# Kernel tuning notes

Hardware: AMD Instinct MI355X
Metric: run time of the kernel (lower is better)

The kernel has to match this reference:

```python
import jax, jax.numpy as jnp
import numpy as np

N, E, DIN, DOUT = 40000, 640000, 128, 256
BN_EPS = 1e-5  # torch BatchNorm1d default eps


def setup_inputs() -> dict:
    key = jax.random.key(0)
    ks = jax.random.split(key, 16)
    x = jax.random.normal(ks[0], (N, DIN), jnp.float32)
    edge_index = jax.random.randint(ks[1], (2, E), 0, N, dtype=jnp.int32)
    s1 = 1.0 / np.sqrt(DIN)
    s2 = 1.0 / np.sqrt(DOUT)
    return {
        "x": x,
        "edge_index": edge_index,
        "eps": jnp.zeros((), jnp.float32),  # GINConv train_eps init = 0
        "W1": jax.random.normal(ks[2], (DIN, DOUT), jnp.float32) * s1,
        "b1": jnp.zeros((DOUT,), jnp.float32),
        "g1": jnp.ones((DOUT,), jnp.float32),
        "bt1": jnp.zeros((DOUT,), jnp.float32),
        "m1": jax.random.normal(ks[3], (DOUT,), jnp.float32) * 0.1,
        "v1": jax.random.uniform(ks[4], (DOUT,), jnp.float32, 0.5, 1.5),
        "W2": jax.random.normal(ks[5], (DOUT, DOUT), jnp.float32) * s2,
        "b2": jnp.zeros((DOUT,), jnp.float32),
        "g2": jnp.ones((DOUT,), jnp.float32),
        "bt2": jnp.zeros((DOUT,), jnp.float32),
        "m2": jax.random.normal(ks[6], (DOUT,), jnp.float32) * 0.1,
        "v2": jax.random.uniform(ks[7], (DOUT,), jnp.float32, 0.5, 1.5),
        "Wres": jax.random.normal(ks[8], (DIN, DOUT), jnp.float32) * s1,
    }


def _bn(h, g, b, m, v):
    # inference-mode BatchNorm1d with running stats
    return (h - m) * jax.lax.rsqrt(v + BN_EPS) * g + b


def reference(x, edge_index, eps, W1, b1, g1, bt1, m1, v1,
              W2, b2, g2, bt2, m2, v2, Wres):
    src, dst = edge_index[0], edge_index[1]
    # GIN sum aggregation: messages x[src] scatter-added at dst
    agg = jax.ops.segment_sum(x[src], dst, num_segments=N)  # [N, DIN]
    h = (1.0 + eps) * x + agg
    h = jax.nn.relu(_bn(h @ W1 + b1, g1, bt1, m1, v1))       # [N, DOUT]
    h = jax.nn.relu(_bn(h @ W2 + b2, g2, bt2, m2, v2))       # [N, DOUT]
    # dropout is identity in eval mode; residual projection since DIN != DOUT
    return jax.nn.relu(h + x @ Wres)
```

## Files before the change

kernel.cpp:

```cpp
#include <hip/hip_runtime.h>

#define NN 40000
#define NPAD 40064
#define EE 640000
#define KDIN 128
#define KDOUT 256

#define NBIN 157
#define BCAP 5120
#define HCAP 2816

typedef __attribute__((ext_vector_type(8))) short bf16x8;
typedef __attribute__((ext_vector_type(4))) float f32x4;

static __device__ __forceinline__ unsigned short f2bf(float f) {
    union { float f; unsigned int u; } v; v.f = f;
    unsigned int r = (v.u + 0x7FFFu + ((v.u >> 16) & 1u)) >> 16;
    return (unsigned short)r;
}
static __device__ __forceinline__ float bf2f(unsigned short h) {
    union { unsigned int u; float f; } v; v.u = ((unsigned int)h) << 16;
    return v.f;
}

#define FRONT_GRID 3177
__global__ __launch_bounds__(256) void k_front(
    const float* __restrict__ x,
    const float* __restrict__ W1, const float* __restrict__ W2,
    const float* __restrict__ Wres, const int* __restrict__ ei,
    ushort* __restrict__ xb, ushort* __restrict__ wt_all,
    unsigned int* __restrict__ recs, int* __restrict__ lmat,
    ushort* __restrict__ hb) {
    __shared__ unsigned int SM[4096 + 480 + 256];
    int b = blockIdx.x, tid = threadIdx.x;
    if (b < NBIN) {
        unsigned int* lrec = SM;
        int* cnt    = (int*)(SM + 4096);
        int* lstart = cnt + 160;
        int* lcur   = lstart + 160;
        int* sw     = lcur + 160;
        int e0 = b * 4096;
        int ns = min(e0 + 4096, EE) - e0;

        if (tid < NBIN) cnt[tid] = 0;
        __syncthreads();
        for (int s = tid; s < ns; s += 256)
            atomicAdd(&cnt[ei[EE + e0 + s] >> 8], 1);
        __syncthreads();
        sw[tid] = (tid < NBIN) ? cnt[tid] : 0;
        __syncthreads();
        for (int off = 1; off < 256; off <<= 1) {
            int add = (tid >= off) ? sw[tid - off] : 0;
            __syncthreads();
            sw[tid] += add;
            __syncthreads();
        }
        if (tid < NBIN) {
            int st = sw[tid] - cnt[tid];
            lstart[tid] = st;
            lcur[tid] = st;
        }
        __syncthreads();
        for (int s = tid; s < ns; s += 256) {
            int e = e0 + s;
            int src = ei[e];
            int dst = ei[EE + e];
            int p = atomicAdd(&lcur[dst >> 8], 1);
            lrec[p] = ((unsigned int)(dst & 255) << 16) | (unsigned int)src;
        }
        __syncthreads();
        for (int s = tid; s < ns; s += 256)
            recs[b * 4096 + s] = lrec[s];
        if (tid < NBIN + 1)
            lmat[b * 158 + tid] = (tid < NBIN) ? lstart[tid] : ns;
    } else if (b < 2661) {
        int i = (b - NBIN) * 256 + tid;
        int row = i >> 4;
        uint4 o = {0, 0, 0, 0};
        if (row < NN) {
            const float4* xp = (const float4*)x + (size_t)i * 2;
            float4 a = xp[0], c = xp[1];
            o.x = (unsigned)f2bf(a.x) | ((unsigned)f2bf(a.y) << 16);
            o.y = (unsigned)f2bf(a.z) | ((unsigned)f2bf(a.w) << 16);
            o.z = (unsigned)f2bf(c.x) | ((unsigned)f2bf(c.y) << 16);
            o.w = (unsigned)f2bf(c.z) | ((unsigned)f2bf(c.w) << 16);
        }
        if (row < NPAD) *(uint4*)(xb + (size_t)i * 8) = o;
    } else if (b < 3173) {
        int j = (b - 2661) * 256 + tid;
        if (j < 32768) {
            int c = j >> 7, r = j & 127;
            wt_all[j] = f2bf(W1[r * KDOUT + c]);
        } else if (j < 98304) {
            int j2 = j - 32768;
            int c = j2 >> 8, r = j2 & 255;
            wt_all[j] = f2bf(W2[r * KDOUT + c]);
        } else {
            int j3 = j - 98304;
            int c = j3 >> 7, r = j3 & 127;
            wt_all[j] = f2bf(Wres[r * KDOUT + c]);
        }
    } else {
        int idx = (b - 3173) * 256 + tid;
        ((uint4*)(hb + (size_t)NN * KDIN))[idx] = (uint4){0, 0, 0, 0};
    }
}

__global__ __launch_bounds__(256) void k_aggD(
    const unsigned int* __restrict__ recs, const int* __restrict__ lmat,
    const ushort* __restrict__ xb, const float* __restrict__ eps,
    ushort* __restrict__ hb) {
    __shared__ unsigned int lrec[BCAP];
    __shared__ ushort lsrc[HCAP];
    __shared__ int lcnt[128], lst[128], lcur[128];
    __shared__ int sw[256];
    int tid = threadIdx.x;
    int bi = blockIdx.x;
    int b = bi >> 3, nh = (bi >> 2) & 1, q = bi & 3;
    int wid = tid >> 6, lane = tid & 63;

    int len0 = 0;
    if (tid < NBIN) len0 = lmat[tid * 158 + b + 1] - lmat[tid * 158 + b];
    sw[tid] = len0;
    __syncthreads();
    for (int off = 1; off < 256; off <<= 1) {
        int add = (tid >= off) ? sw[tid - off] : 0;
        __syncthreads();
        sw[tid] += add;
        __syncthreads();
    }
    int ctot = sw[255];

    for (int c = wid; c < NBIN; c += 4) {
        int s0 = lmat[c * 158 + b];
        int len = lmat[c * 158 + b + 1] - s0;
        int pofs = sw[c] - len;
        const unsigned int* seg = recs + c * 4096 + s0;
        for (int i = lane; i < len; i += 64)
            lrec[pofs + i] = seg[i];
    }
    if (tid < 128) lcnt[tid] = 0;
    __syncthreads();

    for (int s = tid; s < ctot; s += 256) {
        int d8 = lrec[s] >> 16;
        if ((d8 >> 7) == nh) atomicAdd(&lcnt[d8 & 127], 1);
    }
    __syncthreads();
    sw[tid] = (tid < 128) ? lcnt[tid] : 0;
    __syncthreads();
    for (int off = 1; off < 128; off <<= 1) {
        int add = (tid >= off) ? sw[tid - off] : 0;
        __syncthreads();
        sw[tid] += add;
        __syncthreads();
    }
    if (tid < 128) {
        int e = sw[tid] - lcnt[tid];
        lst[tid] = e;
        lcur[tid] = e;
    }
    __syncthreads();
    for (int s = tid; s < ctot; s += 256) {
        unsigned int r = lrec[s];
        int d8 = r >> 16;
        if ((d8 >> 7) == nh) {
            int p = atomicAdd(&lcur[d8 & 127], 1);
            lsrc[p] = (ushort)(r & 0xffff);
        }
    }
    __syncthreads();

    int g = tid >> 2, lane4 = tid & 3;
    float s1 = 1.0f + eps[0];
    for (int it = 0; it < 2; ++it) {
        int d = g + it * 64;
        int node = b * 256 + nh * 128 + d;
        if (node >= NN) continue;
        int st = lst[d], en = st + lcnt[d];
        uint4 me = *((const uint4*)(xb + (size_t)node * KDIN) + q * 4 + lane4);
        float a[8], a2[8];
        a[0] = bf2f((ushort)(me.x & 0xffff)) * s1; a[1] = bf2f((ushort)(me.x >> 16)) * s1;
        a[2] = bf2f((ushort)(me.y & 0xffff)) * s1; a[3] = bf2f((ushort)(me.y >> 16)) * s1;
        a[4] = bf2f((ushort)(me.z & 0xffff)) * s1; a[5] = bf2f((ushort)(me.z >> 16)) * s1;
        a[6] = bf2f((ushort)(me.w & 0xffff)) * s1; a[7] = bf2f((ushort)(me.w >> 16)) * s1;
#pragma unroll
        for (int i = 0; i < 8; ++i) a2[i] = 0.f;
        int e = st;
        for (; e + 1 < en; e += 2) {
            int sA = lsrc[e], sB = lsrc[e + 1];
            uint4 v0 = *((const uint4*)(xb + (size_t)sA * KDIN) + q * 4 + lane4);
            uint4 v1 = *((const uint4*)(xb + (size_t)sB * KDIN) + q * 4 + lane4);
            a[0] += bf2f((ushort)(v0.x & 0xffff)); a[1] += bf2f((ushort)(v0.x >> 16));
            a[2] += bf2f((ushort)(v0.y & 0xffff)); a[3] += bf2f((ushort)(v0.y >> 16));
            a[4] += bf2f((ushort)(v0.z & 0xffff)); a[5] += bf2f((ushort)(v0.z >> 16));
            a[6] += bf2f((ushort)(v0.w & 0xffff)); a[7] += bf2f((ushort)(v0.w >> 16));
            a2[0] += bf2f((ushort)(v1.x & 0xffff)); a2[1] += bf2f((ushort)(v1.x >> 16));
            a2[2] += bf2f((ushort)(v1.y & 0xffff)); a2[3] += bf2f((ushort)(v1.y >> 16));
            a2[4] += bf2f((ushort)(v1.z & 0xffff)); a2[5] += bf2f((ushort)(v1.z >> 16));
            a2[6] += bf2f((ushort)(v1.w & 0xffff)); a2[7] += bf2f((ushort)(v1.w >> 16));
        }
        if (e < en) {
            int sA = lsrc[e];
            uint4 v0 = *((const uint4*)(xb + (size_t)sA * KDIN) + q * 4 + lane4);
            a[0] += bf2f((ushort)(v0.x & 0xffff)); a[1] += bf2f((ushort)(v0.x >> 16));
            a[2] += bf2f((ushort)(v0.y & 0xffff)); a[3] += bf2f((ushort)(v0.y >> 16));
            a[4] += bf2f((ushort)(v0.z & 0xffff)); a[5] += bf2f((ushort)(v0.z >> 16));
            a[6] += bf2f((ushort)(v0.w & 0xffff)); a[7] += bf2f((ushort)(v0.w >> 16));
        }
#pragma unroll
        for (int i = 0; i < 8; ++i) a[i] += a2[i];
        uint4 o;
        o.x = (unsigned)f2bf(a[0]) | ((unsigned)f2bf(a[1]) << 16);
        o.y = (unsigned)f2bf(a[2]) | ((unsigned)f2bf(a[3]) << 16);
        o.z = (unsigned)f2bf(a[4]) | ((unsigned)f2bf(a[5]) << 16);
        o.w = (unsigned)f2bf(a[6]) | ((unsigned)f2bf(a[7]) << 16);
        *((uint4*)(hb + (size_t)node * KDIN) + q * 4 + lane4) = o;
    }
}


#define STAGE_WT(Wt_, Kc_, K2_)                                                 \
    for (int id = tid; id < BNT * (K2_) / 16; id += 256) {                      \
        int c = id / ((K2_) / 16);                                              \
        int koff = (id % ((K2_) / 16)) * 16;                                    \
        uint4 v = *(const uint4*)((const char*)((Wt_) + (size_t)(ncol0 + c) * (Kc_)) + koff); \
        *(uint4*)((char*)s + c * (K2_) + (koff ^ ((c & 7) << 4))) = v;          \
    }

#define MM_LOOP(A_, Kc_, K2_, acc0_, acc1_)                                     \
    {                                                                           \
        const char* a0p = (const char*)((A_) + (size_t)r0 * (Kc_)) + lq * 16;   \
        const char* a1p = a0p + 16 * (Kc_) * 2;                                 \
        for (int k0 = 0; k0 < (Kc_); k0 += 32) {                                \
            bf16x8 a0 = *(const bf16x8*)(a0p + k0 * 2);                         \
            bf16x8 a1 = *(const bf16x8*)(a1p + k0 * 2);                         \
            int kb = (k0 + lq * 8) * 2;                                         \
            _Pragma("unroll")                                                   \
            for (int nt = 0; nt < 8; ++nt) {                                    \
                int c = nt * 16 + l15;                                          \
                bf16x8 b = *(const bf16x8*)((const char*)s + c * (K2_) + (kb ^ ((c & 7) << 4))); \
                acc0_[nt] = __builtin_amdgcn_mfma_f32_16x16x32_bf16(a0, b, acc0_[nt], 0, 0, 0); \
                acc1_[nt] = __builtin_amdgcn_mfma_f32_16x16x32_bf16(a1, b, acc1_[nt], 0, 0, 0); \
            }                                                                   \
        }                                                                       \
    }

#define BNT 128

__global__ __launch_bounds__(256) void k_mm1(
    const ushort* __restrict__ A, const ushort* __restrict__ Wt,
    const float* __restrict__ bb, const float* __restrict__ g,
    const float* __restrict__ bt, const float* __restrict__ m,
    const float* __restrict__ vv, ushort* __restrict__ C) {
    __shared__ ushort s[BNT * 128];
    int tid = threadIdx.x;
    int bm = blockIdx.x >> 1, bn = blockIdx.x & 1;
    int ncol0 = bn * BNT;
    STAGE_WT(Wt, 128, 256);
    __syncthreads();
    int wid = tid >> 6, lane = tid & 63;
    int l15 = lane & 15, lq = lane >> 4;
    int r0 = bm * 128 + wid * 32 + l15;
    f32x4 acc0[8] = {}, acc1[8] = {};
    MM_LOOP(A, 128, 256, acc0, acc1);
#pragma unroll
    for (int nt = 0; nt < 8; ++nt) {
        int col = ncol0 + nt * 16 + l15;
        float sc = g[col] * rsqrtf(vv[col] + 1e-5f);
        float bo = (bb[col] - m[col]) * sc + bt[col];
        int rb = bm * 128 + wid * 32 + lq * 4;
#pragma unroll
        for (int r = 0; r < 4; ++r) {
            C[(size_t)(rb + r) * KDOUT + col] = f2bf(fmaxf(acc0[nt][r] * sc + bo, 0.f));
            C[(size_t)(rb + 16 + r) * KDOUT + col] = f2bf(fmaxf(acc1[nt][r] * sc + bo, 0.f));
        }
    }
}

__global__ __launch_bounds__(256) void k_mm2(
    const ushort* __restrict__ H1, const ushort* __restrict__ W2t,
    const ushort* __restrict__ X, const ushort* __restrict__ Wrt,
    const float* __restrict__ bb, const float* __restrict__ g,
    const float* __restrict__ bt, const float* __restrict__ m,
    const float* __restrict__ vv, float* __restrict__ OUT) {
    __shared__ ushort s[BNT * 256];
    int tid = threadIdx.x;
    int bm = blockIdx.x >> 1, bn = blockIdx.x & 1;
    int ncol0 = bn * BNT;
    int wid = tid >> 6, lane = tid & 63;
    int l15 = lane & 15, lq = lane >> 4;
    int r0 = bm * 128 + wid * 32 + l15;

    STAGE_WT(W2t, 256, 512);
    __syncthreads();
    f32x4 acc0[8] = {}, acc1[8] = {};
    MM_LOOP(H1, 256, 512, acc0, acc1);

    __syncthreads();
    STAGE_WT(Wrt, 128, 256);
    __syncthreads();
    f32x4 acd0[8] = {}, acd1[8] = {};
    MM_LOOP(X, 128, 256, acd0, acd1);

#pragma unroll
    for (int nt = 0; nt < 8; ++nt) {
        int col = ncol0 + nt * 16 + l15;
        float sc = g[col] * rsqrtf(vv[col] + 1e-5f);
        float bo = (bb[col] - m[col]) * sc + bt[col];
        int rb = bm * 128 + wid * 32 + lq * 4;
#pragma unroll
        for (int r = 0; r < 4; ++r) {
            int row0 = rb + r, row1 = rb + 16 + r;
            float t0 = fmaxf(acc0[nt][r] * sc + bo, 0.f);
            float t1 = fmaxf(acc1[nt][r] * sc + bo, 0.f);
            if (row0 < NN) OUT[(size_t)row0 * KDOUT + col] = fmaxf(t0 + acd0[nt][r], 0.f);
            if (row1 < NN) OUT[(size_t)row1 * KDOUT + col] = fmaxf(t1 + acd1[nt][r], 0.f);
        }
    }
}

extern "C" void kernel_launch(void* const* d_in, const int* in_sizes, int n_in,
                              void* d_out, int out_size, void* d_ws, size_t ws_size,
                              hipStream_t stream) {
    const float* x    = (const float*)d_in[0];
    const int*   ei   = (const int*)d_in[1];
    const float* eps  = (const float*)d_in[2];
    const float* W1   = (const float*)d_in[3];
    const float* b1   = (const float*)d_in[4];
    const float* g1   = (const float*)d_in[5];
    const float* bt1  = (const float*)d_in[6];
    const float* m1   = (const float*)d_in[7];
    const float* v1   = (const float*)d_in[8];
    const float* W2   = (const float*)d_in[9];
    const float* b2   = (const float*)d_in[10];
    const float* g2   = (const float*)d_in[11];
    const float* bt2  = (const float*)d_in[12];
    const float* m2   = (const float*)d_in[13];
    const float* v2   = (const float*)d_in[14];
    const float* Wres = (const float*)d_in[15];
    float* out = (float*)d_out;

    char* w = (char*)d_ws;
    ushort* xb  = (ushort*)w;                 w += (size_t)NPAD * KDIN * 2;
    ushort* hb  = (ushort*)w;                 w += (size_t)NPAD * KDIN * 2;
    ushort* h1b = (ushort*)w;                 w += (size_t)NPAD * KDOUT * 2;
    ushort* w1t = (ushort*)w;                 w += 256 * 128 * 2;
    ushort* w2t = (ushort*)w;                 w += 256 * 256 * 2;
    ushort* wrt = (ushort*)w;                 w += 256 * 128 * 2;
    unsigned int* recs = (unsigned int*)w;    w += (size_t)NBIN * 4096 * 4;
    int* lmat   = (int*)w;                    w += (size_t)NBIN * 158 * 4;

    k_front<<<FRONT_GRID, 256, 0, stream>>>(x, W1, W2, Wres, ei, xb, w1t,
                                            recs, lmat, hb);
    k_aggD<<<NBIN * 8, 256, 0, stream>>>(recs, lmat, xb, eps, hb);

    const int grid = (NPAD / 128) * 2;
    k_mm1<<<grid, 256, 0, stream>>>(hb, w1t, b1, g1, bt1, m1, v1, h1b);
    k_mm2<<<grid, 256, 0, stream>>>(h1b, w2t, xb, wrt, b2, g2, bt2, m2, v2, out);
}
```

Baseline: 114.8 us.

## Unroll gather loop by four and use 256-row 512-thread tiles in mm2

The aggregation kernel now keeps four independent source-row loads in flight per iteration instead of two, using macros to trim the repeated code. The second matmul kernel launches 512-thread blocks covering 256 rows each, so the staged weight tile in shared memory is reused by twice as many rows. NPAD and the front-kernel grid are enlarged to match the 256-row tiling. Risks are higher register pressure and fewer blocks in mm2, which may lower occupancy or leave some compute units idle.

```diff
diff --git a/kernel.cpp b/kernel.cpp
--- a/kernel.cpp
+++ b/kernel.cpp
@@ -1,7 +1,7 @@
 #include <hip/hip_runtime.h>
 
 #define NN 40000
-#define NPAD 40064
+#define NPAD 40192
 #define EE 640000
 #define KDIN 128
 #define KDOUT 256
@@ -23,7 +23,7 @@
     return v.f;
 }
 
-#define FRONT_GRID 3177
+#define FRONT_GRID 3193
 __global__ __launch_bounds__(256) void k_front(
     const float* __restrict__ x,
     const float* __restrict__ W1, const float* __restrict__ W2,
@@ -73,7 +73,7 @@
             recs[b * 4096 + s] = lrec[s];
         if (tid < NBIN + 1)
             lmat[b * 158 + tid] = (tid < NBIN) ? lstart[tid] : ns;
-    } else if (b < 2661) {
+    } else if (b < 2669) {
         int i = (b - NBIN) * 256 + tid;
         int row = i >> 4;
         uint4 o = {0, 0, 0, 0};
@@ -85,9 +85,9 @@
             o.z = (unsigned)f2bf(c.x) | ((unsigned)f2bf(c.y) << 16);
             o.w = (unsigned)f2bf(c.z) | ((unsigned)f2bf(c.w) << 16);
         }
-        if (row < NPAD) *(uint4*)(xb + (size_t)i * 8) = o;
-    } else if (b < 3173) {
-        int j = (b - 2661) * 256 + tid;
+        *(uint4*)(xb + (size_t)i * 8) = o;
+    } else if (b < 3181) {
+        int j = (b - 2669) * 256 + tid;
         if (j < 32768) {
             int c = j >> 7, r = j & 127;
             wt_all[j] = f2bf(W1[r * KDOUT + c]);
@@ -101,10 +101,18 @@
             wt_all[j] = f2bf(Wres[r * KDOUT + c]);
         }
     } else {
-        int idx = (b - 3173) * 256 + tid;
+        int idx = (b - 3181) * 256 + tid;
         ((uint4*)(hb + (size_t)NN * KDIN))[idx] = (uint4){0, 0, 0, 0};
     }
 }
+
+#define ACC8(arr_, v_)                                                          \
+    arr_[0] += bf2f((ushort)((v_).x & 0xffff)); arr_[1] += bf2f((ushort)((v_).x >> 16)); \
+    arr_[2] += bf2f((ushort)((v_).y & 0xffff)); arr_[3] += bf2f((ushort)((v_).y >> 16)); \
+    arr_[4] += bf2f((ushort)((v_).z & 0xffff)); arr_[5] += bf2f((ushort)((v_).z >> 16)); \
+    arr_[6] += bf2f((ushort)((v_).w & 0xffff)); arr_[7] += bf2f((ushort)((v_).w >> 16));
+
+#define XROW(n_) (*((const uint4*)(xb + (size_t)(n_) * KDIN) + qoff))
 
 __global__ __launch_bounds__(256) void k_aggD(
     const unsigned int* __restrict__ recs, const int* __restrict__ lmat,
@@ -172,41 +180,35 @@
     __syncthreads();
 
     int g = tid >> 2, lane4 = tid & 3;
+    int qoff = q * 4 + lane4;
     float s1 = 1.0f + eps[0];
     for (int it = 0; it < 2; ++it) {
         int d = g + it * 64;
         int node = b * 256 + nh * 128 + d;
         if (node >= NN) continue;
         int st = lst[d], en = st + lcnt[d];
-        uint4 me = *((const uint4*)(xb + (size_t)node * KDIN) + q * 4 + lane4);
+        uint4 me = XROW(node);
         float a[8], a2[8];
-        a[0] = bf2f((ushort)(me.x & 0xffff)) * s1; a[1] = bf2f((ushort)(me.x >> 16)) * s1;
-        a[2] = bf2f((ushort)(me.y & 0xffff)) * s1; a[3] = bf2f((ushort)(me.y >> 16)) * s1;
-        a[4] = bf2f((ushort)(me.z & 0xffff)) * s1; a[5] = bf2f((ushort)(me.z >> 16)) * s1;
-        a[6] = bf2f((ushort)(me.w & 0xffff)) * s1; a[7] = bf2f((ushort)(me.w >> 16)) * s1;
 #pragma unroll
         for (int i = 0; i < 8; ++i) a2[i] = 0.f;
+        ACC8(a2, me);
+#pragma unroll
+        for (int i = 0; i < 8; ++i) { a[i] = a2[i] * s1; a2[i] = 0.f; }
         int e = st;
-        for (; e + 1 < en; e += 2) {
-            int sA = lsrc[e], sB = lsrc[e + 1];
-            uint4 v0 = *((const uint4*)(xb + (size_t)sA * KDIN) + q * 4 + lane4);
-            uint4 v1 = *((const uint4*)(xb + (size_t)sB * KDIN) + q * 4 + lane4);
-            a[0] += bf2f((ushort)(v0.x & 0xffff)); a[1] += bf2f((ushort)(v0.x >> 16));
-            a[2] += bf2f((ushort)(v0.y & 0xffff)); a[3] += bf2f((ushort)(v0.y >> 16));
-            a[4] += bf2f((ushort)(v0.z & 0xffff)); a[5] += bf2f((ushort)(v0.z >> 16));
-            a[6] += bf2f((ushort)(v0.w & 0xffff)); a[7] += bf2f((ushort)(v0.w >> 16));
-            a2[0] += bf2f((ushort)(v1.x & 0xffff)); a2[1] += bf2f((ushort)(v1.x >> 16));
-            a2[2] += bf2f((ushort)(v1.y & 0xffff)); a2[3] += bf2f((ushort)(v1.y >> 16));
-            a2[4] += bf2f((ushort)(v1.z & 0xffff)); a2[5] += bf2f((ushort)(v1.z >> 16));
-            a2[6] += bf2f((ushort)(v1.w & 0xffff)); a2[7] += bf2f((ushort)(v1.w >> 16));
-        }
-        if (e < en) {
-            int sA = lsrc[e];
-            uint4 v0 = *((const uint4*)(xb + (size_t)sA * KDIN) + q * 4 + lane4);
-            a[0] += bf2f((ushort)(v0.x & 0xffff)); a[1] += bf2f((ushort)(v0.x >> 16));
-            a[2] += bf2f((ushort)(v0.y & 0xffff)); a[3] += bf2f((ushort)(v0.y >> 16));
-            a[4] += bf2f((ushort)(v0.z & 0xffff)); a[5] += bf2f((ushort)(v0.z >> 16));
-            a[6] += bf2f((ushort)(v0.w & 0xffff)); a[7] += bf2f((ushort)(v0.w >> 16));
+        for (; e + 3 < en; e += 4) {
+            int sA = lsrc[e], sB = lsrc[e + 1], sC = lsrc[e + 2], sD = lsrc[e + 3];
+            uint4 v0 = XROW(sA);
+            uint4 v1 = XROW(sB);
+            uint4 v2 = XROW(sC);
+            uint4 v3 = XROW(sD);
+            ACC8(a, v0);
+            ACC8(a2, v1);
+            ACC8(a, v2);
+            ACC8(a2, v3);
+        }
+        for (; e < en; ++e) {
+            uint4 v0 = XROW(lsrc[e]);
+            ACC8(a, v0);
         }
 #pragma unroll
         for (int i = 0; i < 8; ++i) a[i] += a2[i];
@@ -215,13 +217,13 @@
         o.y = (unsigned)f2bf(a[2]) | ((unsigned)f2bf(a[3]) << 16);
         o.z = (unsigned)f2bf(a[4]) | ((unsigned)f2bf(a[5]) << 16);
         o.w = (unsigned)f2bf(a[6]) | ((unsigned)f2bf(a[7]) << 16);
-        *((uint4*)(hb + (size_t)node * KDIN) + q * 4 + lane4) = o;
-    }
-}
-
-
-#define STAGE_WT(Wt_, Kc_, K2_)                                                 \
-    for (int id = tid; id < BNT * (K2_) / 16; id += 256) {                      \
+        *((uint4*)(hb + (size_t)node * KDIN) + qoff) = o;
+    }
+}
+
+
+#define STAGE_WT(Wt_, Kc_, K2_, TPB_)                                           \
+    for (int id = tid; id < BNT * (K2_) / 16; id += (TPB_)) {                   \
         int c = id / ((K2_) / 16);                                              \
         int koff = (id % ((K2_) / 16)) * 16;                                    \
         uint4 v = *(const uint4*)((const char*)((Wt_) + (size_t)(ncol0 + c) * (Kc_)) + koff); \
@@ -257,7 +259,7 @@
     int tid = threadIdx.x;
     int bm = blockIdx.x >> 1, bn = blockIdx.x & 1;
     int ncol0 = bn * BNT;
-    STAGE_WT(Wt, 128, 256);
+    STAGE_WT(Wt, 128, 256, 256);
     __syncthreads();
     int wid = tid >> 6, lane = tid & 63;
     int l15 = lane & 15, lq = lane >> 4;
@@ -278,7 +280,7 @@
     }
 }
 
-__global__ __launch_bounds__(256) void k_mm2(
+__global__ __launch_bounds__(512) void k_mm2(
     const ushort* __restrict__ H1, const ushort* __restrict__ W2t,
     const ushort* __restrict__ X, const ushort* __restrict__ Wrt,
     const float* __restrict__ bb, const float* __restrict__ g,
@@ -290,15 +292,15 @@
     int ncol0 = bn * BNT;
     int wid = tid >> 6, lane = tid & 63;
     int l15 = lane & 15, lq = lane >> 4;
-    int r0 = bm * 128 + wid * 32 + l15;
-
-    STAGE_WT(W2t, 256, 512);
+    int r0 = bm * 256 + wid * 32 + l15;
+
+    STAGE_WT(W2t, 256, 512, 512);
     __syncthreads();
     f32x4 acc0[8] = {}, acc1[8] = {};
     MM_LOOP(H1, 256, 512, acc0, acc1);
 
     __syncthreads();
-    STAGE_WT(Wrt, 128, 256);
+    STAGE_WT(Wrt, 128, 256, 512);
     __syncthreads();
     f32x4 acd0[8] = {}, acd1[8] = {};
     MM_LOOP(X, 128, 256, acd0, acd1);
@@ -308,7 +310,7 @@
         int col = ncol0 + nt * 16 + l15;
         float sc = g[col] * rsqrtf(vv[col] + 1e-5f);
         float bo = (bb[col] - m[col]) * sc + bt[col];
-        int rb = bm * 128 + wid * 32 + lq * 4;
+        int rb = bm * 256 + wid * 32 + lq * 4;
 #pragma unroll
         for (int r = 0; r < 4; ++r) {
             int row0 = rb + r, row1 = rb + 16 + r;
@@ -355,7 +357,7 @@
                                             recs, lmat, hb);
     k_aggD<<<NBIN * 8, 256, 0, stream>>>(recs, lmat, xb, eps, hb);
 
-    const int grid = (NPAD / 128) * 2;
-    k_mm1<<<grid, 256, 0, stream>>>(hb, w1t, b1, g1, bt1, m1, v1, h1b);
-    k_mm2<<<grid, 256, 0, stream>>>(h1b, w2t, xb, wrt, b2, g2, bt2, m2, v2, out);
-}
+    k_mm1<<<(NPAD / 128) * 2, 256, 0, stream>>>(hb, w1t, b1, g1, bt1, m1, v1, h1b);
+    k_mm2<<<(NPAD / 256) * 2, 512, 0, stream>>>(h1b, w2t, xb, wrt, b2, g2, bt2,
+                                                m2, v2, out);
+}
```

After: 109.8 us. 4.3% less time.
